# Performance work log

Measured on AMD Instinct MI355X. Metric: run time of the kernel, lower is better.

Reference implementation:

```python
import jax, jax.numpy as jnp
import numpy as np

BANDWIDTH = 0.1
N_STEPS = 5
TOL = 1e-3
BASE = 3
COORD_OFFSET = 512   # bins assumed within (-512, 511] per dim
COORD_BITS = 10      # 3 dims * 10 bits = 30 bits, fits int32


def _generate_offsets(d, base=3):
    # replicates torch.meshgrid(indexing='ij') over arange(-1, base-1)
    ranges = [np.arange(-1, base - 1) for _ in range(d)]
    mesh = np.meshgrid(*ranges, indexing='ij')
    return jnp.asarray(np.stack(mesh, axis=-1).reshape(-1, d), dtype=jnp.int32)


def _pack_keys(bins):
    # bins: (..., d) int32 -> unique scalar int32 key per bin coordinate
    d = bins.shape[-1]
    key = jnp.zeros(bins.shape[:-1], dtype=jnp.int32)
    for k in range(d):  # tiny fixed loop over dims
        key = (key << COORD_BITS) | (bins[..., k] + COORD_OFFSET)
    return key


def _step(X, offsets, bandwidth):
    # One mean-shift step: bin points, scatter-add sums/counts over the
    # union of offset-shifted bins (torch.unique replaced by exact key
    # packing + sort-based grouping, fixed shapes for jit).
    n, d = X.shape
    m = offsets.shape[0]  # base ** d
    bins = (X / bandwidth).astype(jnp.int32)          # trunc-toward-zero == torch .int()
    shifted = bins[:, None, :] + offsets[None, :, :]  # (n, m, d)
    keys = _pack_keys(shifted).reshape(-1)            # (n*m,)
    K = keys.shape[0]

    order = jnp.argsort(keys)
    skeys = keys[order]
    new_grp = jnp.concatenate(
        [jnp.zeros((1,), jnp.int32), (skeys[1:] != skeys[:-1]).astype(jnp.int32)]
    )
    seg = jnp.cumsum(new_grp)                         # group id per sorted position

    # X repeated once per offset (matches X.repeat(1, m).reshape(-1, d))
    Xflat = jnp.broadcast_to(X[:, None, :], (n, m, d)).reshape(-1, d)
    sum_per = jax.ops.segment_sum(Xflat[order], seg, num_segments=K)          # (K, d)
    cnt_per = jax.ops.segment_sum(jnp.ones((K,), X.dtype), seg, num_segments=K)

    # segment id per original (unsorted) flat position == inverse_indices
    seg_orig = jnp.zeros((K,), seg.dtype).at[order].set(seg)
    sum_mapped = sum_per[seg_orig].reshape(n, m, d).sum(axis=1)   # (n, d)
    cnt_mapped = cnt_per[seg_orig].reshape(n, m).sum(axis=1)      # (n,)
    return sum_mapped / cnt_mapped[:, None]


def setup_inputs() -> dict:
    key = jax.random.key(0)
    X = jax.random.normal(key, (200000, 3), dtype=jnp.float32)
    return {"X": X}


def reference(X):
    n, d = X.shape
    offsets = _generate_offsets(d, BASE)

    def body(carry, _):
        Xc, done = carry
        Xn = _step(Xc, offsets, BANDWIDTH)
        Xn = jnp.where(done, Xc, Xn)  # freeze once converged (== early break)
        conv = jnp.max(jnp.linalg.norm(Xn - Xc, axis=1)) <= TOL
        return (Xn, done | conv), None

    (Xout, _), _ = jax.lax.scan(body, (X, jnp.array(False)), None, length=N_STEPS)
    return Xout
```

## Files before the change

### kernel.cpp

```cpp
#include <hip/hip_runtime.h>


constexpr float BW   = 0.1f;
constexpr float TOL2 = 1e-6f;
constexpr int DIM  = 112, OFF = 56;
constexpr int DIM2 = DIM * DIM;
constexpr int CELLS = DIM * DIM * DIM;
constexpr int CLW = CELLS / 32;
constexpr int RDIM = 16, RC = 7;
constexpr int NREG = RDIM * RDIM * RDIM;
constexpr int RC3 = RC * RC * RC;
constexpr int NB_A = 128, BLK = 256;
constexpr int NF = 2048;
constexpr int IPB = 51;
constexpr float FPS = 16777216.0f;
constexpr double FPSI = 1.0 / 16777216.0;

typedef float vf2 __attribute__((ext_vector_type(2)));

__device__ __forceinline__ int clampb(int v) { return v < 0 ? 0 : (v > DIM - 1 ? DIM - 1 : v); }
__device__ __forceinline__ int binf(float v) { return clampb((int)(v / BW) + OFF); }
__device__ __forceinline__ int flatb(int bx, int by, int bz) { return (bx * DIM + by) * DIM + bz; }
__device__ __forceinline__ int regOf(int bx, int by, int bz) {
    return ((bx / RC) * RDIM + (by / RC)) * RDIM + (bz / RC);
}
__device__ __forceinline__ int lcOf(int bx, int by, int bz) {
    return ((bx % RC) * RC + (by % RC)) * RC + (bz % RC);
}

__device__ __forceinline__ void pk_add(float* p, float a, float b) {
#if defined(__has_builtin) && __has_builtin(__builtin_amdgcn_global_atomic_fadd_v2f32)
    vf2 v = {a, b};
    __builtin_amdgcn_global_atomic_fadd_v2f32((vf2*)p, v);
#else
    atomicAdd(p, a);
    atomicAdd(p + 1, b);
#endif
}

__launch_bounds__(BLK)
__global__ void k_histA(const float* __restrict__ X, int n, int* __restrict__ blockHist,
                        float4* __restrict__ zeroA, float4* __restrict__ zeroB) {
    __shared__ int h[NREG];
    for (int i = threadIdx.x; i < NREG; i += blockDim.x) h[i] = 0;
    __syncthreads();
    int stride = gridDim.x * blockDim.x;
    for (int i = blockIdx.x * blockDim.x + threadIdx.x; i < n; i += stride) {
        float x = X[3 * i + 0], y = X[3 * i + 1], z = X[3 * i + 2];
        atomicAdd(&h[regOf(binf(x), binf(y), binf(z))], 1);
    }
    __syncthreads();
    for (int i = threadIdx.x; i < NREG; i += blockDim.x)
        blockHist[blockIdx.x * NREG + i] = h[i];
    for (int i = blockIdx.x * blockDim.x + threadIdx.x; i < CELLS; i += stride) {
        zeroA[i] = make_float4(0.f, 0.f, 0.f, 0.f);
        zeroB[i] = make_float4(0.f, 0.f, 0.f, 0.f);
    }
}

__global__ void k_colscan(int* __restrict__ blockHist, int* __restrict__ regionPS) {
    int r = blockIdx.x * blockDim.x + threadIdx.x;
    if (r >= NREG) return;
    int run = 0;
    for (int b = 0; b < NB_A; ++b) {
        int idx = b * NREG + r;
        int v = blockHist[idx];
        blockHist[idx] = run;
        run += v;
    }
    regionPS[r] = run;
}

__launch_bounds__(1024)
__global__ void k_regprefix(int* __restrict__ regionPS) {
    __shared__ int buf[1024];
    int t = threadIdx.x;
    int v0 = regionPS[4 * t + 0], v1 = regionPS[4 * t + 1];
    int v2 = regionPS[4 * t + 2], v3 = regionPS[4 * t + 3];
    int s = v0 + v1 + v2 + v3;
    buf[t] = s;
    __syncthreads();
    for (int d = 1; d < 1024; d <<= 1) {
        int add = (t >= d) ? buf[t - d] : 0;
        __syncthreads();
        buf[t] += add;
        __syncthreads();
    }
    int excl = buf[t] - s;
    regionPS[4 * t + 0] = excl;
    regionPS[4 * t + 1] = excl + v0;
    regionPS[4 * t + 2] = excl + v0 + v1;
    regionPS[4 * t + 3] = excl + v0 + v1 + v2;
    if (t == 1023) regionPS[4096] = buf[1023];
}

__launch_bounds__(BLK)
__global__ void k_scatterA(const float* __restrict__ X, int n,
                           const int* __restrict__ blockHist,
                           const int* __restrict__ regionPS,
                           float4* __restrict__ bucket, float4* __restrict__ zeroC) {
    __shared__ int cur[NREG];
    for (int i = threadIdx.x; i < NREG; i += blockDim.x) cur[i] = 0;
    __syncthreads();
    int stride = gridDim.x * blockDim.x;
    for (int i = blockIdx.x * blockDim.x + threadIdx.x; i < n; i += stride) {
        float x = X[3 * i + 0], y = X[3 * i + 1], z = X[3 * i + 2];
        int r = regOf(binf(x), binf(y), binf(z));
        int pos = regionPS[r] + blockHist[blockIdx.x * NREG + r] + atomicAdd(&cur[r], 1);
        bucket[pos] = make_float4(x, y, z, __int_as_float(i));
    }
    for (int i = blockIdx.x * blockDim.x + threadIdx.x; i < CELLS; i += stride)
        zeroC[i] = make_float4(0.f, 0.f, 0.f, 0.f);
}

__launch_bounds__(BLK)
__global__ void k_binB(const float4* __restrict__ bucket, const int* __restrict__ regionPS,
                       float4* __restrict__ A, int* __restrict__ E0,
                       int* __restrict__ PIdx, int* __restrict__ gM0) {
    __shared__ unsigned long long aX[RC3], aY[RC3], aZ[RC3];
    __shared__ unsigned aC[RC3];
    __shared__ int cidx[RC3];
    __shared__ int cnt, cur, sBase;
    int r = blockIdx.x;
    for (int c = threadIdx.x; c < RC3; c += blockDim.x) {
        aX[c] = 0ull; aY[c] = 0ull; aZ[c] = 0ull; aC[c] = 0u;
    }
    if (threadIdx.x == 0) { cnt = 0; cur = 0; }
    __syncthreads();
    int start = regionPS[r], end = regionPS[r + 1];
    for (int i = start + threadIdx.x; i < end; i += blockDim.x) {
        float4 p = bucket[i];
        int lc = lcOf(binf(p.x), binf(p.y), binf(p.z));
        atomicAdd(&aX[lc], (unsigned long long)(long long)rintf(p.x * FPS));
        atomicAdd(&aY[lc], (unsigned long long)(long long)rintf(p.y * FPS));
        atomicAdd(&aZ[lc], (unsigned long long)(long long)rintf(p.z * FPS));
        atomicAdd(&aC[lc], 1u);
    }
    __syncthreads();
    int myc = 0;
    for (int c = threadIdx.x; c < RC3; c += blockDim.x)
        if (aC[c] > 0u) ++myc;
    if (myc) atomicAdd(&cnt, myc);
    __syncthreads();
    if (threadIdx.x == 0 && cnt > 0) sBase = atomicAdd(gM0, cnt);
    __syncthreads();
    int rx = r / (RDIM * RDIM), ry = (r / RDIM) % RDIM, rz = r % RDIM;
    for (int c = threadIdx.x; c < RC3; c += blockDim.x) {
        if (aC[c] > 0u) {
            int idx = sBase + atomicAdd(&cur, 1);
            cidx[c] = idx;
            int bx = rx * RC + c / (RC * RC);
            int by = ry * RC + (c / RC) % RC;
            int bz = rz * RC + c % RC;
            int b = flatb(bx, by, bz);
            E0[idx] = b;
            A[b] = make_float4((float)((double)(long long)aX[c] * FPSI),
                               (float)((double)(long long)aY[c] * FPSI),
                               (float)((double)(long long)aZ[c] * FPSI),
                               (float)aC[c]);
        }
    }
    __syncthreads();
    for (int i = start + threadIdx.x; i < end; i += blockDim.x) {
        float4 p = bucket[i];
        int lc = lcOf(binf(p.x), binf(p.y), binf(p.z));
        PIdx[__float_as_int(p.w)] = cidx[lc];
    }
}

__launch_bounds__(BLK)
__global__ void k_compactM(unsigned* __restrict__ mask, int* __restrict__ listOut,
                           int* __restrict__ pKout) {
    __shared__ int scan[BLK];
    __shared__ int sBase;
    int i = blockIdx.x * blockDim.x + threadIdx.x;
    unsigned w = (i < CLW) ? mask[i] : 0u;
    if (i < CLW && w) mask[i] = 0u;
    int c = __popc(w);
    scan[threadIdx.x] = c;
    __syncthreads();
    for (int d = 1; d < BLK; d <<= 1) {
        int add = (threadIdx.x >= (unsigned)d) ? scan[threadIdx.x - d] : 0;
        __syncthreads();
        scan[threadIdx.x] += add;
        __syncthreads();
    }
    if (threadIdx.x == BLK - 1) {
        int tot = scan[BLK - 1];
        sBase = tot ? atomicAdd(pKout, tot) : 0;
    }
    __syncthreads();
    int base = sBase + scan[threadIdx.x] - c;
    int bb = i * 32;
    while (w) {
        int b = __ffs(w) - 1;
        listOut[base++] = bb + b;
        w &= w - 1;
    }
}

__launch_bounds__(BLK)
__global__ void k_fused(
    const float4* __restrict__ src, const int* __restrict__ list, const int* __restrict__ pK,
    float4* __restrict__ REo, int* __restrict__ IDXo, float4* __restrict__ eposInit,
    float4* __restrict__ tgt, unsigned* __restrict__ clT,
    int updS, const float* __restrict__ X, int n, const int* __restrict__ PIdx,
    const float4* __restrict__ REp, const int* __restrict__ IDXp,
    const int* __restrict__ pM0, float4* __restrict__ epos,
    unsigned* __restrict__ notConv,
    const int* __restrict__ clearList, const int* __restrict__ pKc,
    float4* __restrict__ clearGrid, int lastStep) {
    __shared__ float4 sh[BLK];
    __shared__ unsigned sFlag;
    if (threadIdx.x == 0) sFlag = 0;
    __syncthreads();
    int K = *pK;
    int NC = (K + IPB - 1) / IPB;
    int BC = NC;
    if (BC > NF - 256) BC = NF - 256;
    const float t5[5] = {1.f, 2.f, 3.f, 2.f, 1.f};
    bool moved = false;

    if ((int)blockIdx.x < BC) {
        int first, last, step;
        if (BC >= 64) {
            int xcd = blockIdx.x & 7, loc = blockIdx.x >> 3;
            int cpx = (NC + 7) >> 3;
            int bpx = ((BC - 1 - xcd) >> 3) + 1;
            first = xcd * cpx + loc;
            last = (xcd + 1) * cpx; if (last > NC) last = NC;
            step = bpx;
        } else {
            first = blockIdx.x; last = NC; step = BC;
        }
        for (int ib = first; ib < last; ib += step) {
            int li = threadIdx.x / 5;
            int dx = threadIdx.x % 5;
            int item = ib * IPB + li;
            float4 part = make_float4(0.f, 0.f, 0.f, 0.f);
            if (li < IPB && item < K) {
                int b = list[item];
                int bx = b / DIM2, rem = b % DIM2;
                int by = rem / DIM, bz = rem % DIM;
                int ix = bx + dx - 2;
                if ((unsigned)ix < (unsigned)DIM) {
                    float wx = t5[dx];
                    if (by >= 2 && by <= DIM - 3 && bz >= 2 && bz <= DIM - 3) {
                        #pragma unroll
                        for (int dy = 0; dy < 5; ++dy) {
                            float wxy = wx * t5[dy];
                            const float4* row = src + flatb(ix, by + dy - 2, bz - 2);
                            #pragma unroll
                            for (int dz = 0; dz < 5; ++dz) {
                                float w = wxy * t5[dz];
                                float4 e = row[dz];
                                part.x = fmaf(w, e.x, part.x);
                                part.y = fmaf(w, e.y, part.y);
                                part.z = fmaf(w, e.z, part.z);
                                part.w = fmaf(w, e.w, part.w);
                            }
                        }
                    } else {
                        for (int dy = 0; dy < 5; ++dy) {
                            int iy = by + dy - 2;
                            if ((unsigned)iy >= (unsigned)DIM) continue;
                            float wxy = wx * t5[dy];
                            for (int dz = 0; dz < 5; ++dz) {
                                int iz = bz + dz - 2;
                                if ((unsigned)iz >= (unsigned)DIM) continue;
                                float w = wxy * t5[dz];
                                float4 e = src[flatb(ix, iy, iz)];
                                part.x = fmaf(w, e.x, part.x);
                                part.y = fmaf(w, e.y, part.y);
                                part.z = fmaf(w, e.z, part.z);
                                part.w = fmaf(w, e.w, part.w);
                            }
                        }
                    }
                }
            }
            sh[threadIdx.x] = part;
            __syncthreads();
            if (threadIdx.x < 64) {
                int item2 = ib * IPB + threadIdx.x;
                bool valid = (threadIdx.x < IPB) && (item2 < K);
                int bn = -1;
                float4 sv = make_float4(0.f, 0.f, 0.f, 0.f);
                if (valid) {
                    int base5 = threadIdx.x * 5;
                    float4 a0 = sh[base5 + 0], a1 = sh[base5 + 1], a2 = sh[base5 + 2];
                    float4 a3 = sh[base5 + 3], a4 = sh[base5 + 4];
                    float sx = a0.x + a1.x + a2.x + a3.x + a4.x;
                    float sy = a0.y + a1.y + a2.y + a3.y + a4.y;
                    float sz = a0.z + a1.z + a2.z + a3.z + a4.z;
                    float sc = a0.w + a1.w + a2.w + a3.w + a4.w;
                    int b = list[item2];
                    float W = src[b].w;
                    float4 np = make_float4(sx / sc, sy / sc, sz / sc, W);
                    REo[item2] = np;
                    IDXo[b] = item2;
                    if (eposInit) eposInit[item2] = np;
                    if (!lastStep) {
                        bn = flatb(binf(np.x), binf(np.y), binf(np.z));
                        sv = make_float4(W * np.x, W * np.y, W * np.z, W);
                    }
                }
                if (!lastStep) {
                    int pbn = __shfl_up(bn, 1, 64);
                    unsigned f = (threadIdx.x == 0 || pbn != bn) ? 1u : 0u;
                    unsigned nf = __shfl_down(f, 1, 64);
                    bool leader = valid && (threadIdx.x == 63 || nf != 0u);
                    #pragma unroll
                    for (int off = 1; off < 64; off <<= 1) {
                        float ox = __shfl_up(sv.x, off, 64);
                        float oy = __shfl_up(sv.y, off, 64);
                        float oz = __shfl_up(sv.z, off, 64);
                        float ow = __shfl_up(sv.w, off, 64);
                        unsigned of = __shfl_up(f, off, 64);
                        if ((int)threadIdx.x >= off) {
                            if (!f) { sv.x += ox; sv.y += oy; sv.z += oz; sv.w += ow; }
                            f |= of;
                        }
                    }
                    if (leader) {
                        float* cell = (float*)&tgt[bn];
                        pk_add(cell + 0, sv.x, sv.y);
                        pk_add(cell + 2, sv.z, sv.w);
                        atomicOr(&clT[(unsigned)bn >> 5], 1u << (bn & 31));
                    }
                }
            }
            __syncthreads();
        }
    } else {
        int U = (updS > 0) ? (X ? n : *pM0) : 0;
        int CL = clearList ? *pKc : 0;
        int total = U + CL;
        bool done = false;
        if (updS > 1) {
            for (int t = 1; t < updS; ++t) done |= (notConv[t] == 0u);
        }
        int stride = (NF - BC) * blockDim.x;
        for (int idx = (blockIdx.x - BC) * blockDim.x + threadIdx.x; idx < total;
             idx += stride) {
            if (idx < U) {
                int e = idx;
                if (X) {
                    float x = X[3 * e + 0], y = X[3 * e + 1], z = X[3 * e + 2];
                    float4 rr = REp[PIdx[e]];
                    float ex = rr.x - x, ey = rr.y - y, ez = rr.z - z;
                    moved |= (fmaf(ex, ex, fmaf(ey, ey, ez * ez)) > TOL2);
                } else if (!done) {
                    float4 p = epos[e];
                    int j = IDXp[flatb(binf(p.x), binf(p.y), binf(p.z))];
                    float4 rr = REp[j];
                    float ex = rr.x - p.x, ey = rr.y - p.y, ez = rr.z - p.z;
                    moved |= (fmaf(ex, ex, fmaf(ey, ey, ez * ez)) > TOL2);
                    epos[e] = make_float4(rr.x, rr.y, rr.z, p.w);
                }
            } else {
                clearGrid[clearList[idx - U]] = make_float4(0.f, 0.f, 0.f, 0.f);
            }
        }
    }
    if (moved) sFlag = 1;
    __syncthreads();
    if (threadIdx.x == 0 && updS > 0 && sFlag) notConv[updS] = 1u;
}

__launch_bounds__(BLK)
__global__ void k_fin(const float4* __restrict__ REa, const int* __restrict__ IDXa,
                      const float4* __restrict__ epos, const int* __restrict__ pM0,
                      const unsigned* __restrict__ notConv, float4* __restrict__ fpos) {
    int M0 = *pM0;
    bool done = false;
    for (int t = 1; t <= 4; ++t) done |= (notConv[t] == 0u);
    for (int e = blockIdx.x * blockDim.x + threadIdx.x; e < M0;
         e += gridDim.x * blockDim.x) {
        float4 p = epos[e];
        if (!done) {
            float4 rr = REa[IDXa[flatb(binf(p.x), binf(p.y), binf(p.z))]];
            p.x = rr.x; p.y = rr.y; p.z = rr.z;
        }
        fpos[e] = p;
    }
}

__global__ void k_map(const int* __restrict__ PIdx, int n, const float4* __restrict__ fpos,
                      float* __restrict__ out) {
    int i = blockIdx.x * blockDim.x + threadIdx.x;
    if (i >= n) return;
    float4 p = fpos[PIdx[i]];
    out[3 * i + 0] = p.x;
    out[3 * i + 1] = p.y;
    out[3 * i + 2] = p.z;
}

extern "C" void kernel_launch(void* const* d_in, const int* in_sizes, int n_in,
                              void* d_out, int out_size, void* d_ws, size_t ws_size,
                              hipStream_t stream) {
    const float* X = (const float*)d_in[0];
    int n = in_sizes[0] / 3;

    char* ws = (char*)d_ws;
    int*      cnt     = (int*)ws;
    unsigned* notConv = (unsigned*)(ws + 32);
    size_t mB = (size_t)CLW * 4;
    size_t gB = (size_t)CELLS * 16;
    unsigned* m0 = (unsigned*)(ws + 256);
    unsigned* m1 = (unsigned*)(ws + 256 + mB);
    float4* A = (float4*)(ws + 256 + 2 * mB);
    float4* B = (float4*)((char*)A + gB);
    float4* C = (float4*)((char*)B + gB);
    int* IDXa = (int*)((char*)C + gB);
    int* IDXb = IDXa + CELLS;
    float4* REa  = (float4*)(IDXb + CELLS);
    float4* REb  = REa + n;
    float4* epos = REb + n;
    int* E0   = (int*)(epos + n);
    int* La   = E0 + n;
    int* Lb   = La + n;
    int* Lc   = Lb + n;
    int* Ld   = Lc + n;
    int* PIdx = Ld + n;
    float4* bucket = (float4*)(PIdx + n);
    int* blockHist = (int*)(bucket + n);
    int* regionPS  = blockHist + NB_A * NREG;

    hipMemsetAsync(ws, 0, 256 + 2 * mB, stream);

    const int NCM = (CLW + BLK - 1) / BLK;

    k_histA<<<NB_A, BLK, 0, stream>>>(X, n, blockHist, A, B);
    k_colscan<<<NREG / BLK, BLK, 0, stream>>>(blockHist, regionPS);
    k_regprefix<<<1, 1024, 0, stream>>>(regionPS);
    k_scatterA<<<NB_A, BLK, 0, stream>>>(X, n, blockHist, regionPS, bucket, C);
    k_binB<<<NREG, BLK, 0, stream>>>(bucket, regionPS, A, E0, PIdx, &cnt[1]);

    k_fused<<<NF, BLK, 0, stream>>>(A, E0, &cnt[1], REa, IDXa, epos,
                                    B, m0,
                                    0, nullptr, n, nullptr, nullptr, nullptr, nullptr,
                                    nullptr, notConv, nullptr, nullptr, nullptr, 0);
    k_compactM<<<NCM, BLK, 0, stream>>>(m0, La, &cnt[2]);
    k_fused<<<NF, BLK, 0, stream>>>(B, La, &cnt[2], REb, IDXb, nullptr,
                                    C, m1,
                                    1, X, n, PIdx, REa, IDXa, &cnt[1], nullptr,
                                    notConv, E0, &cnt[1], A, 0);
    k_compactM<<<NCM, BLK, 0, stream>>>(m1, Lb, &cnt[3]);
    k_fused<<<NF, BLK, 0, stream>>>(C, Lb, &cnt[3], REa, IDXa, nullptr,
                                    A, m0,
                                    2, nullptr, n, nullptr, REb, IDXb, &cnt[1], epos,
                                    notConv, La, &cnt[2], B, 0);
    k_compactM<<<NCM, BLK, 0, stream>>>(m0, Lc, &cnt[4]);
    k_fused<<<NF, BLK, 0, stream>>>(A, Lc, &cnt[4], REb, IDXb, nullptr,
                                    B, m1,
                                    3, nullptr, n, nullptr, REa, IDXa, &cnt[1], epos,
                                    notConv, nullptr, nullptr, nullptr, 0);
    k_compactM<<<NCM, BLK, 0, stream>>>(m1, Ld, &cnt[5]);
    k_fused<<<NF, BLK, 0, stream>>>(B, Ld, &cnt[5], REa, IDXa, nullptr,
                                    nullptr, nullptr,
                                    4, nullptr, n, nullptr, REb, IDXb, &cnt[1], epos,
                                    notConv, nullptr, nullptr, nullptr, 1);

    k_fin<<<256, BLK, 0, stream>>>(REa, IDXa, epos, &cnt[1], notConv, REb);
    k_map<<<(n + BLK - 1) / BLK, BLK, 0, stream>>>(PIdx, n, REb, (float*)d_out);
}
```

Measured before the change: 246.5 us.

## Replace occupancy bitmask atomics with grid-scan compaction and fuse final gather into map

```diff
diff --git a/kernel.cpp b/kernel.cpp
--- a/kernel.cpp
+++ b/kernel.cpp
@@ -6,13 +6,14 @@
 constexpr int DIM  = 112, OFF = 56;
 constexpr int DIM2 = DIM * DIM;
 constexpr int CELLS = DIM * DIM * DIM;
-constexpr int CLW = CELLS / 32;
 constexpr int RDIM = 16, RC = 7;
 constexpr int NREG = RDIM * RDIM * RDIM;
 constexpr int RC3 = RC * RC * RC;
 constexpr int NB_A = 128, BLK = 256;
 constexpr int NF = 2048;
 constexpr int IPB = 51;
+constexpr int CPT = 32;
+constexpr int NBG = (CELLS + BLK * CPT - 1) / (BLK * CPT);
 constexpr float FPS = 16777216.0f;
 constexpr double FPSI = 1.0 / 16777216.0;
 
@@ -169,41 +170,10 @@
 }
 
 __launch_bounds__(BLK)
-__global__ void k_compactM(unsigned* __restrict__ mask, int* __restrict__ listOut,
-                           int* __restrict__ pKout) {
-    __shared__ int scan[BLK];
-    __shared__ int sBase;
-    int i = blockIdx.x * blockDim.x + threadIdx.x;
-    unsigned w = (i < CLW) ? mask[i] : 0u;
-    if (i < CLW && w) mask[i] = 0u;
-    int c = __popc(w);
-    scan[threadIdx.x] = c;
-    __syncthreads();
-    for (int d = 1; d < BLK; d <<= 1) {
-        int add = (threadIdx.x >= (unsigned)d) ? scan[threadIdx.x - d] : 0;
-        __syncthreads();
-        scan[threadIdx.x] += add;
-        __syncthreads();
-    }
-    if (threadIdx.x == BLK - 1) {
-        int tot = scan[BLK - 1];
-        sBase = tot ? atomicAdd(pKout, tot) : 0;
-    }
-    __syncthreads();
-    int base = sBase + scan[threadIdx.x] - c;
-    int bb = i * 32;
-    while (w) {
-        int b = __ffs(w) - 1;
-        listOut[base++] = bb + b;
-        w &= w - 1;
-    }
-}
-
-__launch_bounds__(BLK)
 __global__ void k_fused(
     const float4* __restrict__ src, const int* __restrict__ list, const int* __restrict__ pK,
     float4* __restrict__ REo, int* __restrict__ IDXo, float4* __restrict__ eposInit,
-    float4* __restrict__ tgt, unsigned* __restrict__ clT,
+    float4* __restrict__ tgt,
     int updS, const float* __restrict__ X, int n, const int* __restrict__ PIdx,
     const float4* __restrict__ REp, const int* __restrict__ IDXp,
     const int* __restrict__ pM0, float4* __restrict__ epos,
@@ -326,7 +296,6 @@
                         float* cell = (float*)&tgt[bn];
                         pk_add(cell + 0, sv.x, sv.y);
                         pk_add(cell + 2, sv.z, sv.w);
-                        atomicOr(&clT[(unsigned)bn >> 5], 1u << (bn & 31));
                     }
                 }
             }
@@ -369,28 +338,50 @@
 }
 
 __launch_bounds__(BLK)
-__global__ void k_fin(const float4* __restrict__ REa, const int* __restrict__ IDXa,
-                      const float4* __restrict__ epos, const int* __restrict__ pM0,
-                      const unsigned* __restrict__ notConv, float4* __restrict__ fpos) {
-    int M0 = *pM0;
+__global__ void k_compactG(const float4* __restrict__ G, int* __restrict__ listOut,
+                           int* __restrict__ pKout) {
+    __shared__ int scan[BLK];
+    __shared__ int sBase;
+    const float* __restrict__ Gw = (const float*)G;
+    int base = (blockIdx.x * BLK + threadIdx.x) * CPT;
+    int c = 0;
+    #pragma unroll 4
+    for (int k = 0; k < CPT; ++k) {
+        int i = base + k;
+        if (i < CELLS && Gw[4 * i + 3] > 0.f) ++c;
+    }
+    scan[threadIdx.x] = c;
+    __syncthreads();
+    for (int d = 1; d < BLK; d <<= 1) {
+        int add = (threadIdx.x >= (unsigned)d) ? scan[threadIdx.x - d] : 0;
+        __syncthreads();
+        scan[threadIdx.x] += add;
+        __syncthreads();
+    }
+    if (threadIdx.x == BLK - 1) {
+        int tot = scan[BLK - 1];
+        sBase = tot ? atomicAdd(pKout, tot) : 0;
+    }
+    __syncthreads();
+    int pos = sBase + scan[threadIdx.x] - c;
+    for (int k = 0; k < CPT; ++k) {
+        int i = base + k;
+        if (i < CELLS && Gw[4 * i + 3] > 0.f) listOut[pos++] = i;
+    }
+}
+
+__global__ void k_map(const int* __restrict__ PIdx, int n, const float4* __restrict__ epos,
+                      const float4* __restrict__ REa, const int* __restrict__ IDXa,
+                      const unsigned* __restrict__ notConv, float* __restrict__ out) {
     bool done = false;
     for (int t = 1; t <= 4; ++t) done |= (notConv[t] == 0u);
-    for (int e = blockIdx.x * blockDim.x + threadIdx.x; e < M0;
-         e += gridDim.x * blockDim.x) {
-        float4 p = epos[e];
-        if (!done) {
-            float4 rr = REa[IDXa[flatb(binf(p.x), binf(p.y), binf(p.z))]];
-            p.x = rr.x; p.y = rr.y; p.z = rr.z;
-        }
-        fpos[e] = p;
-    }
-}
-
-__global__ void k_map(const int* __restrict__ PIdx, int n, const float4* __restrict__ fpos,
-                      float* __restrict__ out) {
     int i = blockIdx.x * blockDim.x + threadIdx.x;
     if (i >= n) return;
-    float4 p = fpos[PIdx[i]];
+    float4 p = epos[PIdx[i]];
+    if (!done) {
+        float4 rr = REa[IDXa[flatb(binf(p.x), binf(p.y), binf(p.z))]];
+        p.x = rr.x; p.y = rr.y; p.z = rr.z;
+    }
     out[3 * i + 0] = p.x;
     out[3 * i + 1] = p.y;
     out[3 * i + 2] = p.z;
@@ -405,11 +396,8 @@
     char* ws = (char*)d_ws;
     int*      cnt     = (int*)ws;
     unsigned* notConv = (unsigned*)(ws + 32);
-    size_t mB = (size_t)CLW * 4;
     size_t gB = (size_t)CELLS * 16;
-    unsigned* m0 = (unsigned*)(ws + 256);
-    unsigned* m1 = (unsigned*)(ws + 256 + mB);
-    float4* A = (float4*)(ws + 256 + 2 * mB);
+    float4* A = (float4*)(ws + 256);
     float4* B = (float4*)((char*)A + gB);
     float4* C = (float4*)((char*)B + gB);
     int* IDXa = (int*)((char*)C + gB);
@@ -427,9 +415,7 @@
     int* blockHist = (int*)(bucket + n);
     int* regionPS  = blockHist + NB_A * NREG;
 
-    hipMemsetAsync(ws, 0, 256 + 2 * mB, stream);
-
-    const int NCM = (CLW + BLK - 1) / BLK;
+    hipMemsetAsync(ws, 0, 256, stream);
 
     k_histA<<<NB_A, BLK, 0, stream>>>(X, n, blockHist, A, B);
     k_colscan<<<NREG / BLK, BLK, 0, stream>>>(blockHist, regionPS);
@@ -438,30 +424,30 @@
     k_binB<<<NREG, BLK, 0, stream>>>(bucket, regionPS, A, E0, PIdx, &cnt[1]);
 
     k_fused<<<NF, BLK, 0, stream>>>(A, E0, &cnt[1], REa, IDXa, epos,
-                                    B, m0,
+                                    B,
                                     0, nullptr, n, nullptr, nullptr, nullptr, nullptr,
                                     nullptr, notConv, nullptr, nullptr, nullptr, 0);
-    k_compactM<<<NCM, BLK, 0, stream>>>(m0, La, &cnt[2]);
+    k_compactG<<<NBG, BLK, 0, stream>>>(B, La, &cnt[2]);
     k_fused<<<NF, BLK, 0, stream>>>(B, La, &cnt[2], REb, IDXb, nullptr,
-                                    C, m1,
+                                    C,
                                     1, X, n, PIdx, REa, IDXa, &cnt[1], nullptr,
                                     notConv, E0, &cnt[1], A, 0);
-    k_compactM<<<NCM, BLK, 0, stream>>>(m1, Lb, &cnt[3]);
+    k_compactG<<<NBG, BLK, 0, stream>>>(C, Lb, &cnt[3]);
     k_fused<<<NF, BLK, 0, stream>>>(C, Lb, &cnt[3], REa, IDXa, nullptr,
-                                    A, m0,
+                                    A,
                                     2, nullptr, n, nullptr, REb, IDXb, &cnt[1], epos,
                                     notConv, La, &cnt[2], B, 0);
-    k_compactM<<<NCM, BLK, 0, stream>>>(m0, Lc, &cnt[4]);
+    k_compactG<<<NBG, BLK, 0, stream>>>(A, Lc, &cnt[4]);
     k_fused<<<NF, BLK, 0, stream>>>(A, Lc, &cnt[4], REb, IDXb, nullptr,
-                                    B, m1,
+                                    B,
                                     3, nullptr, n, nullptr, REa, IDXa, &cnt[1], epos,
                                     notConv, nullptr, nullptr, nullptr, 0);
-    k_compactM<<<NCM, BLK, 0, stream>>>(m1, Ld, &cnt[5]);
+    k_compactG<<<NBG, BLK, 0, stream>>>(B, Ld, &cnt[5]);
     k_fused<<<NF, BLK, 0, stream>>>(B, Ld, &cnt[5], REa, IDXa, nullptr,
-                                    nullptr, nullptr,
+                                    nullptr,
                                     4, nullptr, n, nullptr, REb, IDXb, &cnt[1], epos,
                                     notConv, nullptr, nullptr, nullptr, 1);
 
-    k_fin<<<256, BLK, 0, stream>>>(REa, IDXa, epos, &cnt[1], notConv, REb);
-    k_map<<<(n + BLK - 1) / BLK, BLK, 0, stream>>>(PIdx, n, REb, (float*)d_out);
-}
+    k_map<<<(n + BLK - 1) / BLK, BLK, 0, stream>>>(PIdx, n, epos, REa, IDXa,
+                                                   notConv, (float*)d_out);
+}
```

Measured after the change: 281.1 us. +14.0%, slower.
